# Kernel tuning notes

Hardware: AMD Instinct MI355X
Metric: run time of the kernel (lower is better)

Reference implementation:

```python
import jax, jax.numpy as jnp
import numpy as np

OUT_F, IN_F = 8192, 4096
TOKENS = 512


def _unpack_int2_to_ternary(packed, alpha, dtype):
    # packed: [out_f, in_f//4] ints 0..255; 4 two-bit codes per byte.
    # code 0 -> -1, code 2 -> +1, codes 1/3 -> 0; then scale by per-row alpha.
    shifts = jnp.arange(4, dtype=packed.dtype) * 2  # [0,2,4,6]
    two_bit = (packed[:, :, None] >> shifts[None, None, :]) & 3  # [out_f, in_f//4, 4]
    two_bit = two_bit.reshape(packed.shape[0], -1)  # [out_f, in_f]
    sign = jnp.where(two_bit == 2, 1.0, jnp.where(two_bit == 0, -1.0, 0.0)).astype(dtype)
    return sign * alpha.astype(dtype)[:, None]


def setup_inputs() -> dict:
    key = jax.random.key(0)
    k1, k2, k3, k4 = jax.random.split(key, 4)
    x = jax.random.normal(k1, (TOKENS, IN_F), dtype=jnp.float32)
    weight_int2 = jax.random.randint(k2, (OUT_F, IN_F // 4), 0, 256, dtype=jnp.int32)
    alpha = jax.random.uniform(k3, (OUT_F,), dtype=jnp.float32, minval=0.01, maxval=0.05)
    bias = jax.random.normal(k4, (OUT_F,), dtype=jnp.float32) * 0.01
    return {"x": x, "weight_int2": weight_int2, "alpha": alpha, "bias": bias}


def reference(x, weight_int2, alpha, bias):
    W = _unpack_int2_to_ternary(weight_int2, alpha, x.dtype)  # [out_f, in_f]
    out = x @ W.T  # [tokens, out_f]
    return out + bias
```

## Files before the change

### kernel.cpp

```cpp
#include <hip/hip_runtime.h>
#include <hip/hip_bf16.h>

typedef unsigned int u32;
typedef unsigned short u16;

#define TOKENS 512
#define OUT_F  8192
#define IN_F   4096
#define KPACK  (IN_F / 4)
#define TMB 128
#define TNB 128
#define BKW 256
#define NWIN (IN_F / BKW)

typedef __attribute__((ext_vector_type(8))) short bf16x8;
typedef __attribute__((ext_vector_type(4))) float f32x4;
typedef __attribute__((ext_vector_type(16))) float f32x16;

__device__ __forceinline__ u32 pack_bf16x2(float a, float b) {
    __hip_bfloat162 h = __float22bfloat162_rn(make_float2(a, b));
    union { __hip_bfloat162 h2; u32 u; } cvt;
    cvt.h2 = h;
    return cvt.u;
}

__device__ __forceinline__ u32 decode_pair(u32 d) {
    u32 s = (__umul24(d, 0x808202u) & 0x06060606u) + 0x01000100u;
    return __builtin_amdgcn_perm(0x00003F80u, 0x0000BF80u, s);
}
__device__ __forceinline__ bf16x8 decode_frag(u32 w, int sh) {
    union { bf16x8 v; u32 u[4]; } c;
    c.u[0] = decode_pair((w >> (sh + 0)) & 0xFu);
    c.u[1] = decode_pair((w >> (sh + 4)) & 0xFu);
    c.u[2] = decode_pair((w >> (sh + 8)) & 0xFu);
    c.u[3] = decode_pair((w >> (sh + 12)) & 0xFu);
    return c.v;
}

__device__ __forceinline__ void async_ld16(const void* g, void* l) {
    __builtin_amdgcn_global_load_lds(
        (const __attribute__((address_space(1))) u32*)g,
        (__attribute__((address_space(3))) u32*)l, 16, 0, 0);
}

__device__ __forceinline__ void async_b4(const uint4* g, uint4& dst) {
    asm volatile("global_load_dwordx4 %0, %1, off"
                 : "=v"(dst) : "v"(g) : "memory");
}

#define VMW(N) asm volatile("s_waitcnt vmcnt(" #N ")" ::: "memory")

__global__ __launch_bounds__(256) void prep(const float* __restrict__ X,
                                            u16* __restrict__ Xb,
                                            const u32* __restrict__ W2,
                                            uint4* __restrict__ W10) {
    __shared__ u32 dense[128 * 32];
    const int t = threadIdx.x;

    if (blockIdx.y == 8) {
        int base = blockIdx.x * 32768 + t * 8;
#pragma unroll
        for (int r = 0; r < 16; ++r) {
            int i = base + r * 2048;
            float4 a = *(const float4*)(X + i);
            float4 b = *(const float4*)(X + i + 4);
            uint4 q;
            q.x = pack_bf16x2(a.x, a.y);
            q.y = pack_bf16x2(a.z, a.w);
            q.z = pack_bf16x2(b.x, b.y);
            q.w = pack_bf16x2(b.z, b.w);
            *(uint4*)(Xb + i) = q;
        }
        return;
    }

    const int ngrp = blockIdx.x;
    const int kc   = blockIdx.y;
#pragma unroll
    for (int i = 0; i < 16; ++i) {
        int id = t + 256 * i;
        int col = id >> 5, jq = id & 31;
        uint4 wv = *(const uint4*)(W2 + (size_t)(ngrp * 128 + col) * KPACK + kc * 128 + jq * 4);
        dense[col * 32 + (jq ^ (col & 31))] =
            (wv.x & 0xFFu) | ((wv.y & 0xFFu) << 8) | ((wv.z & 0xFFu) << 16) | ((wv.w & 0xFFu) << 24);
    }
    __syncthreads();
    const u16* sp = (const u16*)dense;
#pragma unroll
    for (int p = 0; p < 4; ++p) {
        int e = t + 256 * p;
        int lane = e & 63;
        int kq = (e >> 6) & 3;
        int nh = (e >> 8) & 1;
        int wloc = (e >> 9) & 1;
        int h = lane >> 5;
        int c0 = nh * 64 + (lane & 31), c1 = c0 + 32;
        u32 f[4], g[4];
#pragma unroll
        for (int ks = 0; ks < 4; ++ks) {
            int j = wloc * 16 + kq * 4 + ks;
            f[ks] = sp[((c0 * 32 + (j ^ (c0 & 31))) << 1) | h];
            g[ks] = sp[((c1 * 32 + (j ^ (c1 & 31))) << 1) | h];
        }
        uint4 o;
        o.x = f[0] | (f[1] << 16);
        o.y = f[2] | (f[3] << 16);
        o.z = g[0] | (g[1] << 16);
        o.w = g[2] | (g[3] << 16);
        int w = kc * 2 + wloc;
        W10[(((size_t)(ngrp * 2 + nh) * 4 + kq) * NWIN + w) * 64 + lane] = o;
    }
}

__global__ __launch_bounds__(512, 2) void ternary_gemm14(
    const u16* __restrict__ Xb,
    const uint4* __restrict__ W10,
    const float* __restrict__ alpha,
    const float* __restrict__ bias,
    float* __restrict__ Out)
{
    __shared__ u16 As[2][TMB * BKW];

    const int tid  = threadIdx.x;
    const int lane = tid & 63;
    const int wave = tid >> 6;
    const int kq = wave & 3;
    const int nh = wave >> 2;

    const int m0 = blockIdx.x * TMB;
    const int ngrp = blockIdx.y;
    const int n0 = ngrp * TNB;

    f32x16 acc[4][2];
#pragma unroll
    for (int mt = 0; mt < 4; ++mt)
#pragma unroll
        for (int nt = 0; nt < 2; ++nt)
#pragma unroll
            for (int i = 0; i < 16; ++i)
                acc[mt][nt][i] = 0.f;

    const u16* gbase = Xb + (size_t)(m0 + wave * 16) * IN_F;
    u32 aoff[8];
    u32 lbase[8];
#pragma unroll
    for (int i = 0; i < 8; ++i) {
        int rr = i * 2 + (lane >> 5);
        int cd = ((lane & 15) ^ (rr & 15)) | (lane & 16);
        aoff[i] = rr * IN_F + cd * 8;
        lbase[i] = (wave * 16 + i * 2) * BKW;
    }

    u32 ofsA0[4];
#pragma unroll
    for (int ks = 0; ks < 4; ++ks) {
        int row = lane & 31;
        int chunk = kq * 8 + ks * 2 + (lane >> 5);
        int slot = ((chunk & 15) ^ (row & 15)) | (chunk & 16);
        ofsA0[ks] = row * BKW + slot * 8;
    }

    const uint4* wq = W10 + (((size_t)(ngrp * 2 + nh) * 4 + kq) * NWIN) * 64 + lane;

    auto issueA = [&](int w) {
        u16* d = As[w & 1];
        const int koff = w * BKW;
#pragma unroll
        for (int i = 0; i < 8; ++i)
            async_ld16(gbase + aoff[i] + koff, d + lbase[i]);
    };

    auto window_compute = [&](int buf, uint4 bq) {
        const u16* ab = As[buf];
#pragma unroll
        for (int ks = 0; ks < 4; ++ks) {
            const u16* ap = ab + ofsA0[ks];
            bf16x8 a0 = *(const bf16x8*)(ap);
            bf16x8 a1 = *(const bf16x8*)(ap + 8192);
            bf16x8 a2 = *(const bf16x8*)(ap + 16384);
            bf16x8 a3 = *(const bf16x8*)(ap + 24576);
            u32 wx = (ks < 2) ? bq.x : bq.y;
            u32 wz = (ks < 2) ? bq.z : bq.w;
            const int sh = (ks & 1) * 16;
            bf16x8 b0 = decode_frag(wx, sh);
            bf16x8 b1 = decode_frag(wz, sh);
            acc[0][0] = __builtin_amdgcn_mfma_f32_32x32x16_bf16(a0, b0, acc[0][0], 0, 0, 0);
            acc[1][0] = __builtin_amdgcn_mfma_f32_32x32x16_bf16(a1, b0, acc[1][0], 0, 0, 0);
            acc[2][0] = __builtin_amdgcn_mfma_f32_32x32x16_bf16(a2, b0, acc[2][0], 0, 0, 0);
            acc[3][0] = __builtin_amdgcn_mfma_f32_32x32x16_bf16(a3, b0, acc[3][0], 0, 0, 0);
            acc[0][1] = __builtin_amdgcn_mfma_f32_32x32x16_bf16(a0, b1, acc[0][1], 0, 0, 0);
            acc[1][1] = __builtin_amdgcn_mfma_f32_32x32x16_bf16(a1, b1, acc[1][1], 0, 0, 0);
            acc[2][1] = __builtin_amdgcn_mfma_f32_32x32x16_bf16(a2, b1, acc[2][1], 0, 0, 0);
            acc[3][1] = __builtin_amdgcn_mfma_f32_32x32x16_bf16(a3, b1, acc[3][1], 0, 0, 0);
        }
    };

    uint4 bqE, bqO;
    async_b4(wq, bqE);
    issueA(0);
    async_b4(wq + 64, bqO);

#pragma unroll 1
    for (int p = 0; p < (NWIN - 2) / 2; ++p) {
        const int w = 2 * p;
        VMW(1);
        __builtin_amdgcn_s_barrier();
        __builtin_amdgcn_sched_barrier(0);
        issueA(w + 1);
        window_compute(0, bqE);
        async_b4(wq + (size_t)(w + 2) * 64, bqE);

        VMW(1);
        __builtin_amdgcn_s_barrier();
        __builtin_amdgcn_sched_barrier(0);
        issueA(w + 2);
        window_compute(1, bqO);
        async_b4(wq + (size_t)(w + 3) * 64, bqO);
    }
    VMW(1);
    __builtin_amdgcn_s_barrier();
    __builtin_amdgcn_sched_barrier(0);
    issueA(15);
    window_compute(0, bqE);
    VMW(0);
    __builtin_amdgcn_s_barrier();
    __builtin_amdgcn_sched_barrier(0);
    window_compute(1, bqO);

    f32x4* red = (f32x4*)As;
#pragma unroll 1
    for (int q = 1; q < 4; ++q) {
        if (kq == q) {
            f32x4* dst = red + nh * 2048 + lane;
#pragma unroll
            for (int mt = 0; mt < 4; ++mt)
#pragma unroll
                for (int nt = 0; nt < 2; ++nt)
#pragma unroll
                    for (int sub = 0; sub < 4; ++sub) {
                        f32x4 v = {acc[mt][nt][sub * 4 + 0], acc[mt][nt][sub * 4 + 1],
                                   acc[mt][nt][sub * 4 + 2], acc[mt][nt][sub * 4 + 3]};
                        dst[(mt * 8 + nt * 4 + sub) * 64] = v;
                    }
        }
        __syncthreads();
        if (kq == 0) {
            const f32x4* src = red + nh * 2048 + lane;
#pragma unroll
            for (int mt = 0; mt < 4; ++mt)
#pragma unroll
                for (int nt = 0; nt < 2; ++nt)
#pragma unroll
                    for (int sub = 0; sub < 4; ++sub) {
                        f32x4 v = src[(mt * 8 + nt * 4 + sub) * 64];
#pragma unroll
                        for (int i = 0; i < 4; ++i)
                            acc[mt][nt][sub * 4 + i] += v[i];
                    }
        }
        __syncthreads();
    }

    if (kq == 0) {
#pragma unroll
        for (int nt = 0; nt < 2; ++nt) {
            int ncol = n0 + nh * 64 + nt * 32 + (lane & 31);
            float av = alpha[ncol];
            float bv = bias[ncol];
#pragma unroll
            for (int mt = 0; mt < 4; ++mt) {
#pragma unroll
                for (int r = 0; r < 16; ++r) {
                    int row = m0 + mt * 32 + (r & 3) + 8 * (r >> 2) + 4 * (lane >> 5);
                    Out[(size_t)row * OUT_F + ncol] = acc[mt][nt][r] * av + bv;
                }
            }
        }
    }
}

__global__ void ternary_naive(const float* __restrict__ X, const u32* __restrict__ W2,
                              const float* __restrict__ alpha, const float* __restrict__ bias,
                              float* __restrict__ Out) {
    int o  = blockIdx.x * 64 + (threadIdx.x & 63);
    int tk = blockIdx.y * 4 + (threadIdx.x >> 6);
    const float* x = X + (size_t)tk * IN_F;
    const u32* w = W2 + (size_t)o * KPACK;
    float s = 0.f;
    for (int d = 0; d < KPACK; ++d) {
        u32 b = w[d] & 0xFFu;
        const float* xp = x + d * 4;
#pragma unroll
        for (int j = 0; j < 4; ++j) {
            u32 c = (b >> (2 * j)) & 3u;
            float wv = (c == 2u) ? 1.f : ((c == 0u) ? -1.f : 0.f);
            s += xp[j] * wv;
        }
    }
    Out[(size_t)tk * OUT_F + o] = s * alpha[o] + bias[o];
}

extern "C" void kernel_launch(void* const* d_in, const int* in_sizes, int n_in,
                              void* d_out, int out_size, void* d_ws, size_t ws_size,
                              hipStream_t stream) {
    const float* x = (const float*)d_in[0];
    const u32* w2 = (const u32*)d_in[1];
    const float* alpha = (const float*)d_in[2];
    const float* bias  = (const float*)d_in[3];
    float* out = (float*)d_out;

    const size_t xb_bytes  = (size_t)TOKENS * IN_F * sizeof(u16);
    const size_t w10_bytes = (size_t)OUT_F * IN_F / 4;

    if (ws_size >= xb_bytes + w10_bytes) {
        u16* xb = (u16*)d_ws;
        uint4* w10 = (uint4*)((char*)d_ws + xb_bytes);
        prep<<<dim3(64, 9), 256, 0, stream>>>(x, xb, w2, w10);
        ternary_gemm14<<<dim3(TOKENS / TMB, OUT_F / TNB), 512, 0, stream>>>(xb, w10, alpha, bias, out);
    } else {
        ternary_naive<<<dim3(OUT_F / 64, TOKENS / 4), 256, 0, stream>>>(x, w2, alpha, bias, out);
    }
}
```

Before: 126.5 us.

## Split waves along M instead of N so each wave decodes all N columns

Reassigns the two wave halves from splitting the N dimension to splitting the M dimension, so each wave computes a 64x128 tile with 2 M-tiles by 4 N-tiles. The packed weight layout is reordered so both N halves of a k-quarter sit contiguously, and each wave now loads two weight vectors per window. This halves LDS A-fragment reads per wave but doubles the ternary decode work per wave, trading LDS bandwidth for more VALU decode and more global weight loads.

```diff
diff --git a/kernel.cpp b/kernel.cpp
--- a/kernel.cpp
+++ b/kernel.cpp
@@ -53,7 +53,7 @@
 __global__ __launch_bounds__(256) void prep(const float* __restrict__ X,
                                             u16* __restrict__ Xb,
                                             const u32* __restrict__ W2,
-                                            uint4* __restrict__ W10) {
+                                            uint4* __restrict__ W11) {
     __shared__ u32 dense[128 * 32];
     const int t = threadIdx.x;
 
@@ -91,10 +91,10 @@
         int e = t + 256 * p;
         int lane = e & 63;
         int kq = (e >> 6) & 3;
-        int nh = (e >> 8) & 1;
+        int half = (e >> 8) & 1;
         int wloc = (e >> 9) & 1;
         int h = lane >> 5;
-        int c0 = nh * 64 + (lane & 31), c1 = c0 + 32;
+        int c0 = half * 64 + (lane & 31), c1 = c0 + 32;
         u32 f[4], g[4];
 #pragma unroll
         for (int ks = 0; ks < 4; ++ks) {
@@ -108,13 +108,13 @@
         o.z = g[0] | (g[1] << 16);
         o.w = g[2] | (g[3] << 16);
         int w = kc * 2 + wloc;
-        W10[(((size_t)(ngrp * 2 + nh) * 4 + kq) * NWIN + w) * 64 + lane] = o;
-    }
-}
-
-__global__ __launch_bounds__(512, 2) void ternary_gemm14(
+        W11[((size_t)(ngrp * 4 + kq) * NWIN + w) * 128 + half * 64 + lane] = o;
+    }
+}
+
+__global__ __launch_bounds__(512, 2) void ternary_gemm15(
     const u16* __restrict__ Xb,
-    const uint4* __restrict__ W10,
+    const uint4* __restrict__ W11,
     const float* __restrict__ alpha,
     const float* __restrict__ bias,
     float* __restrict__ Out)
@@ -125,17 +125,17 @@
     const int lane = tid & 63;
     const int wave = tid >> 6;
     const int kq = wave & 3;
-    const int nh = wave >> 2;
+    const int mh = wave >> 2;
 
     const int m0 = blockIdx.x * TMB;
     const int ngrp = blockIdx.y;
     const int n0 = ngrp * TNB;
 
-    f32x16 acc[4][2];
-#pragma unroll
-    for (int mt = 0; mt < 4; ++mt)
-#pragma unroll
-        for (int nt = 0; nt < 2; ++nt)
+    f32x16 acc[2][4];
+#pragma unroll
+    for (int mt = 0; mt < 2; ++mt)
+#pragma unroll
+        for (int nt = 0; nt < 4; ++nt)
 #pragma unroll
             for (int i = 0; i < 16; ++i)
                 acc[mt][nt][i] = 0.f;
@@ -154,13 +154,13 @@
     u32 ofsA0[4];
 #pragma unroll
     for (int ks = 0; ks < 4; ++ks) {
-        int row = lane & 31;
+        int row = mh * 64 + (lane & 31);
         int chunk = kq * 8 + ks * 2 + (lane >> 5);
         int slot = ((chunk & 15) ^ (row & 15)) | (chunk & 16);
         ofsA0[ks] = row * BKW + slot * 8;
     }
 
-    const uint4* wq = W10 + (((size_t)(ngrp * 2 + nh) * 4 + kq) * NWIN) * 64 + lane;
+    const uint4* wq = W11 + ((size_t)(ngrp * 4 + kq) * NWIN) * 128 + lane;
 
     auto issueA = [&](int w) {
         u16* d = As[w & 1];
@@ -169,90 +169,92 @@
         for (int i = 0; i < 8; ++i)
             async_ld16(gbase + aoff[i] + koff, d + lbase[i]);
     };
-
-    auto window_compute = [&](int buf, uint4 bq) {
+    auto issueB = [&](int w, uint4& qa, uint4& qb) {
+        const uint4* p = wq + (size_t)w * 128;
+        async_b4(p, qa);
+        async_b4(p + 64, qb);
+    };
+
+    auto window_compute = [&](int buf, uint4 qa, uint4 qb) {
         const u16* ab = As[buf];
 #pragma unroll
         for (int ks = 0; ks < 4; ++ks) {
             const u16* ap = ab + ofsA0[ks];
             bf16x8 a0 = *(const bf16x8*)(ap);
             bf16x8 a1 = *(const bf16x8*)(ap + 8192);
-            bf16x8 a2 = *(const bf16x8*)(ap + 16384);
-            bf16x8 a3 = *(const bf16x8*)(ap + 24576);
-            u32 wx = (ks < 2) ? bq.x : bq.y;
-            u32 wz = (ks < 2) ? bq.z : bq.w;
             const int sh = (ks & 1) * 16;
-            bf16x8 b0 = decode_frag(wx, sh);
-            bf16x8 b1 = decode_frag(wz, sh);
-            acc[0][0] = __builtin_amdgcn_mfma_f32_32x32x16_bf16(a0, b0, acc[0][0], 0, 0, 0);
-            acc[1][0] = __builtin_amdgcn_mfma_f32_32x32x16_bf16(a1, b0, acc[1][0], 0, 0, 0);
-            acc[2][0] = __builtin_amdgcn_mfma_f32_32x32x16_bf16(a2, b0, acc[2][0], 0, 0, 0);
-            acc[3][0] = __builtin_amdgcn_mfma_f32_32x32x16_bf16(a3, b0, acc[3][0], 0, 0, 0);
-            acc[0][1] = __builtin_amdgcn_mfma_f32_32x32x16_bf16(a0, b1, acc[0][1], 0, 0, 0);
-            acc[1][1] = __builtin_amdgcn_mfma_f32_32x32x16_bf16(a1, b1, acc[1][1], 0, 0, 0);
-            acc[2][1] = __builtin_amdgcn_mfma_f32_32x32x16_bf16(a2, b1, acc[2][1], 0, 0, 0);
-            acc[3][1] = __builtin_amdgcn_mfma_f32_32x32x16_bf16(a3, b1, acc[3][1], 0, 0, 0);
+#pragma unroll
+            for (int nt = 0; nt < 4; ++nt) {
+                u32 f;
+                if      (nt == 0) f = (ks < 2) ? qa.x : qa.y;
+                else if (nt == 1) f = (ks < 2) ? qa.z : qa.w;
+                else if (nt == 2) f = (ks < 2) ? qb.x : qb.y;
+                else              f = (ks < 2) ? qb.z : qb.w;
+                bf16x8 b = decode_frag(f, sh);
+                acc[0][nt] = __builtin_amdgcn_mfma_f32_32x32x16_bf16(a0, b, acc[0][nt], 0, 0, 0);
+                acc[1][nt] = __builtin_amdgcn_mfma_f32_32x32x16_bf16(a1, b, acc[1][nt], 0, 0, 0);
+            }
         }
     };
 
-    uint4 bqE, bqO;
-    async_b4(wq, bqE);
+    uint4 bqEa, bqEb, bqOa, bqOb;
+    issueB(0, bqEa, bqEb);
     issueA(0);
-    async_b4(wq + 64, bqO);
+    issueB(1, bqOa, bqOb);
 
 #pragma unroll 1
     for (int p = 0; p < (NWIN - 2) / 2; ++p) {
         const int w = 2 * p;
-        VMW(1);
+        VMW(2);
         __builtin_amdgcn_s_barrier();
         __builtin_amdgcn_sched_barrier(0);
         issueA(w + 1);
-        window_compute(0, bqE);
-        async_b4(wq + (size_t)(w + 2) * 64, bqE);
-
-        VMW(1);
+        window_compute(0, bqEa, bqEb);
+        issueB(w + 2, bqEa, bqEb);
+
+        VMW(2);
         __builtin_amdgcn_s_barrier();
         __builtin_amdgcn_sched_barrier(0);
         issueA(w + 2);
-        window_compute(1, bqO);
-        async_b4(wq + (size_t)(w + 3) * 64, bqO);
-    }
-    VMW(1);
+        window_compute(1, bqOa, bqOb);
+        issueB(w + 3, bqOa, bqOb);
+    }
+    VMW(2);
     __builtin_amdgcn_s_barrier();
     __builtin_amdgcn_sched_barrier(0);
     issueA(15);
-    window_compute(0, bqE);
+    window_compute(0, bqEa, bqEb);
     VMW(0);
     __builtin_amdgcn_s_barrier();
     __builtin_amdgcn_sched_barrier(0);
-    window_compute(1, bqO);
+    window_compute(1, bqOa, bqOb);
 
     f32x4* red = (f32x4*)As;
 #pragma unroll 1
     for (int q = 1; q < 4; ++q) {
         if (kq == q) {
-            f32x4* dst = red + nh * 2048 + lane;
-#pragma unroll
-            for (int mt = 0; mt < 4; ++mt)
-#pragma unroll
-                for (int nt = 0; nt < 2; ++nt)
+            f32x4* dst = red + mh * 2048 + lane;
+#pragma unroll
+            for (int mt = 0; mt < 2; ++mt)
+#pragma unroll
+                for (int nt = 0; nt < 4; ++nt)
 #pragma unroll
                     for (int sub = 0; sub < 4; ++sub) {
                         f32x4 v = {acc[mt][nt][sub * 4 + 0], acc[mt][nt][sub * 4 + 1],
                                    acc[mt][nt][sub * 4 + 2], acc[mt][nt][sub * 4 + 3]};
-                        dst[(mt * 8 + nt * 4 + sub) * 64] = v;
+                        dst[(mt * 16 + nt * 4 + sub) * 64] = v;
                     }
         }
         __syncthreads();
         if (kq == 0) {
-            const f32x4* src = red + nh * 2048 + lane;
-#pragma unroll
-            for (int mt = 0; mt < 4; ++mt)
-#pragma unroll
-                for (int nt = 0; nt < 2; ++nt)
+            const f32x4* src = red + mh * 2048 + lane;
+#pragma unroll
+            for (int mt = 0; mt < 2; ++mt)
+#pragma unroll
+                for (int nt = 0; nt < 4; ++nt)
 #pragma unroll
                     for (int sub = 0; sub < 4; ++sub) {
-                        f32x4 v = src[(mt * 8 + nt * 4 + sub) * 64];
+                        f32x4 v = src[(mt * 16 + nt * 4 + sub) * 64];
 #pragma unroll
                         for (int i = 0; i < 4; ++i)
                             acc[mt][nt][sub * 4 + i] += v[i];
@@ -263,15 +265,15 @@
 
     if (kq == 0) {
 #pragma unroll
-        for (int nt = 0; nt < 2; ++nt) {
-            int ncol = n0 + nh * 64 + nt * 32 + (lane & 31);
+        for (int nt = 0; nt < 4; ++nt) {
+            int ncol = n0 + nt * 32 + (lane & 31);
             float av = alpha[ncol];
             float bv = bias[ncol];
 #pragma unroll
-            for (int mt = 0; mt < 4; ++mt) {
+            for (int mt = 0; mt < 2; ++mt) {
 #pragma unroll
                 for (int r = 0; r < 16; ++r) {
-                    int row = m0 + mt * 32 + (r & 3) + 8 * (r >> 2) + 4 * (lane >> 5);
+                    int row = m0 + mh * 64 + mt * 32 + (r & 3) + 8 * (r >> 2) + 4 * (lane >> 5);
                     Out[(size_t)row * OUT_F + ncol] = acc[mt][nt][r] * av + bv;
                 }
             }
@@ -310,13 +312,13 @@
     float* out = (float*)d_out;
 
     const size_t xb_bytes  = (size_t)TOKENS * IN_F * sizeof(u16);
-    const size_t w10_bytes = (size_t)OUT_F * IN_F / 4;
-
-    if (ws_size >= xb_bytes + w10_bytes) {
+    const size_t w11_bytes = (size_t)OUT_F * IN_F / 4;
+
+    if (ws_size >= xb_bytes + w11_bytes) {
         u16* xb = (u16*)d_ws;
-        uint4* w10 = (uint4*)((char*)d_ws + xb_bytes);
-        prep<<<dim3(64, 9), 256, 0, stream>>>(x, xb, w2, w10);
-        ternary_gemm14<<<dim3(TOKENS / TMB, OUT_F / TNB), 512, 0, stream>>>(xb, w10, alpha, bias, out);
+        uint4* w11 = (uint4*)((char*)d_ws + xb_bytes);
+        prep<<<dim3(64, 9), 256, 0, stream>>>(x, xb, w2, w11);
+        ternary_gemm15<<<dim3(TOKENS / TMB, OUT_F / TNB), 512, 0, stream>>>(xb, w11, alpha, bias, out);
     } else {
         ternary_naive<<<dim3(OUT_F / 64, TOKENS / 4), 256, 0, stream>>>(x, w2, alpha, bias, out);
     }
```

Result: slower. 133.1 us (+5.2%).
